# Kernel tuning notes

Measured on AMD Instinct MI355X. Metric: run time of the kernel, lower is better.

## Reference

```python
import jax, jax.numpy as jnp
import numpy as np

# --- constants mirroring init_kwargs ---
DIM = 1024
N_HEADS = 16
N_KV_HEADS = 4
HEAD_DIM = DIM // N_HEADS          # 64
REP = N_HEADS // N_KV_HEADS        # 4
ROPE_THETA = 10000.0
WINDOW = 512
N_GLOBAL = 64
EPS = 1e-6


def setup_inputs() -> dict:
    key = jax.random.key(0)
    ks = jax.random.split(key, 7)
    B, L = 2, 2048
    x = jax.random.normal(ks[0], (B, L, DIM), dtype=jnp.float32)
    s = 0.02
    wq = jax.random.normal(ks[1], (DIM, N_HEADS * HEAD_DIM), dtype=jnp.float32) * s
    wk = jax.random.normal(ks[2], (DIM, N_KV_HEADS * HEAD_DIM), dtype=jnp.float32) * s
    wv = jax.random.normal(ks[3], (DIM, N_KV_HEADS * HEAD_DIM), dtype=jnp.float32) * s
    wo = jax.random.normal(ks[4], (N_HEADS * HEAD_DIM, DIM), dtype=jnp.float32) * s
    gq = jnp.ones((HEAD_DIM,), dtype=jnp.float32) + 0.01 * jax.random.normal(ks[5], (HEAD_DIM,), dtype=jnp.float32)
    gk = jnp.ones((HEAD_DIM,), dtype=jnp.float32) + 0.01 * jax.random.normal(ks[6], (HEAD_DIM,), dtype=jnp.float32)
    return {"x": x, "wq": wq, "wk": wk, "wv": wv, "wo": wo, "gq": gq, "gk": gk}


def _rmsnorm(t, g):
    # QKNorm: RMS norm over head_dim with learnable per-dim scale
    return t * jax.lax.rsqrt(jnp.mean(t * t, axis=-1, keepdims=True) + EPS) * g


def _rope(t, cos, sin):
    # t: [B,H,L,hd]; complex RoPE over consecutive pairs (2i, 2i+1)
    t1 = t[..., 0::2]
    t2 = t[..., 1::2]
    o1 = t1 * cos - t2 * sin
    o2 = t1 * sin + t2 * cos
    return jnp.stack([o1, o2], axis=-1).reshape(t.shape)


def reference(x, wq, wk, wv, wo, gq, gk):
    B, L, D = x.shape
    q = (x @ wq).reshape(B, L, N_HEADS, HEAD_DIM)
    k = (x @ wk).reshape(B, L, N_KV_HEADS, HEAD_DIM)
    v = (x @ wv).reshape(B, L, N_KV_HEADS, HEAD_DIM)
    q = _rmsnorm(q, gq)
    k = _rmsnorm(k, gk)
    q = q.transpose(0, 2, 1, 3)  # [B,H,L,hd]
    k = k.transpose(0, 2, 1, 3)
    v = v.transpose(0, 2, 1, 3)

    # RoPE frequencies (start_pos = 0)
    inv_freq = 1.0 / (ROPE_THETA ** (jnp.arange(0, HEAD_DIM, 2, dtype=jnp.float32) / HEAD_DIM))
    ang = jnp.arange(L, dtype=jnp.float32)[:, None] * inv_freq[None, :]  # [L, hd/2]
    cos, sin = jnp.cos(ang), jnp.sin(ang)
    q = _rope(q, cos, sin)
    k = _rope(k, cos, sin)

    # GQA: repeat kv heads (repeat_interleave on head dim)
    k = jnp.repeat(k, REP, axis=1)
    v = jnp.repeat(v, REP, axis=1)

    scores = jnp.einsum("bhqd,bhkd->bhqk", q, k) / np.sqrt(HEAD_DIM).astype(np.float32)

    # sliding-window + global-token causal mask
    half = WINDOW // 2
    i = jnp.arange(L)[:, None]
    j = jnp.arange(L)[None, :]
    m = (j <= i) & ((j >= i - half) | (j < N_GLOBAL))  # [L,L] bool
    scores = jnp.where(m[None, None], scores, -jnp.inf)

    attn = jax.nn.softmax(scores.astype(jnp.float32), axis=-1).astype(scores.dtype)
    out = jnp.einsum("bhqk,bhkd->bhqd", attn, v)
    out = out.transpose(0, 2, 1, 3).reshape(B, L, N_HEADS * HEAD_DIM)
    return out @ wo
```

## Files before the change

kernel.cpp:

```cpp
#include <hip/hip_runtime.h>
#include <hip/hip_bf16.h>

typedef __bf16 bf16x8 __attribute__((ext_vector_type(8)));
typedef __bf16 bf16x4 __attribute__((ext_vector_type(4)));
typedef float  f32x4  __attribute__((ext_vector_type(4)));
typedef short  s16x4  __attribute__((ext_vector_type(4)));

__device__ __forceinline__ __bf16 to_bf16(float f) {
    __hip_bfloat16 h = __float2bfloat16(f);
    return *reinterpret_cast<__bf16*>(&h);
}

__device__ __forceinline__ f32x4 mfma32(bf16x8 a, bf16x8 b, f32x4 c) {
    return __builtin_amdgcn_mfma_f32_16x16x32_bf16(a, b, c, 0, 0, 0);
}
__device__ __forceinline__ f32x4 mfma16(bf16x4 a, bf16x4 b, f32x4 c) {
#if __has_builtin(__builtin_amdgcn_mfma_f32_16x16x16_bf16)
    return __builtin_amdgcn_mfma_f32_16x16x16_bf16(a, b, c, 0, 0, 0);
#else
    return __builtin_amdgcn_mfma_f32_16x16x16bf16_1k(
        __builtin_bit_cast(s16x4, a), __builtin_bit_cast(s16x4, b), c, 0, 0, 0);
#endif
}

__device__ __forceinline__ void gload_lds16(const __bf16* g, __bf16* l) {
    __builtin_amdgcn_global_load_lds(
        (const __attribute__((address_space(1))) void*)g,
        (__attribute__((address_space(3))) void*)l, 16, 0, 0);
}


__global__ __launch_bounds__(256) void prep_k(const float* __restrict__ wq,
                                              const float* __restrict__ wk,
                                              const float* __restrict__ wv,
                                              const float* __restrict__ wo,
                                              const float* __restrict__ x,
                                              __bf16* __restrict__ WqkvT,
                                              __bf16* __restrict__ WoT,
                                              __bf16* __restrict__ xb) {
    int b = blockIdx.x, tid = threadIdx.x;
    if (b >= 2560) {
        int i = ((b - 2560) * 256 + tid) * 8;
        f32x4 a = *(const f32x4*)(x + i);
        f32x4 c = *(const f32x4*)(x + i + 4);
        bf16x8 h;
        h[0] = to_bf16(a.x); h[1] = to_bf16(a.y); h[2] = to_bf16(a.z); h[3] = to_bf16(a.w);
        h[4] = to_bf16(c.x); h[5] = to_bf16(c.y); h[6] = to_bf16(c.z); h[7] = to_bf16(c.w);
        *(bf16x8*)(xb + i) = h;
        return;
    }
    __shared__ float tile[32][33];
    const float* src; __bf16* dst; int N, idx;
    if (b < 1024)      { src = wq; dst = WqkvT;                        N = 1024; idx = b; }
    else if (b < 1280) { src = wk; dst = WqkvT + (size_t)1024 * 1024;  N = 256;  idx = b - 1024; }
    else if (b < 1536) { src = wv; dst = WqkvT + (size_t)1280 * 1024;  N = 256;  idx = b - 1280; }
    else               { src = wo; dst = WoT;                          N = 1024; idx = b - 1536; }
    int k0 = (idx & 31) * 32, n0 = (idx >> 5) * 32;
    int tx = tid & 31, ty = tid >> 5;
#pragma unroll
    for (int r = 0; r < 4; ++r) {
        int kk = ty + r * 8;
        tile[kk][tx] = src[(size_t)(k0 + kk) * N + n0 + tx];
    }
    __syncthreads();
#pragma unroll
    for (int r = 0; r < 4; ++r) {
        int nn = ty + r * 8;
        dst[(size_t)(n0 + nn) * 1024 + k0 + tx] = to_bf16(tile[tx][nn]);
    }
}

#define GEMM_CORE(A, BT, K)                                                     \
    __shared__ __bf16 lA[8192];                                                 \
    __shared__ __bf16 lB[4096];                                                 \
    int tid = threadIdx.x;                                                      \
    int m0 = blockIdx.x * 128, n0 = blockIdx.y * 64;                            \
    int wid = tid >> 6, lane = tid & 63;                                        \
    int wm = (wid & 1) * 64, wn = (wid >> 1) * 32;                              \
    int lm = lane & 15, qd = lane >> 4;                                         \
    f32x4 acc[4][2] = {};                                                       \
    for (int k0 = 0; k0 < (K); k0 += 64) {                                      \
        _Pragma("unroll")                                                       \
        for (int it = 0; it < 4; ++it) {                                        \
            int kh = it >> 1, half = it & 1;                                    \
            int c = half * 256 + tid;                                           \
            int row = c >> 2, c4 = c & 3;                                       \
            __bf16* la = lA + kh * 4096 + half * 2048 + wid * 512;              \
            gload_lds16((A) + (size_t)(m0 + row) * (K) + k0 + kh * 32 + c4 * 8, la); \
        }                                                                       \
        _Pragma("unroll")                                                       \
        for (int kh = 0; kh < 2; ++kh) {                                        \
            int row = tid >> 2, c4 = tid & 3;                                   \
            __bf16* lb = lB + kh * 2048 + wid * 512;                            \
            gload_lds16((BT) + (size_t)(n0 + row) * (K) + k0 + kh * 32 + c4 * 8, lb); \
        }                                                                       \
        __syncthreads();                                                        \
        _Pragma("unroll")                                                       \
        for (int kh = 0; kh < 2; ++kh) {                                        \
            bf16x8 af[4], bfr[2];                                               \
            _Pragma("unroll")                                                   \
            for (int t = 0; t < 4; ++t) {                                       \
                int row = wm + t * 16 + lm;                                     \
                af[t] = *(const bf16x8*)&lA[kh * 4096 + (row >> 6) * 2048       \
                                            + (row & 63) * 32 + qd * 8];        \
            }                                                                   \
            _Pragma("unroll")                                                   \
            for (int j = 0; j < 2; ++j)                                         \
                bfr[j] = *(const bf16x8*)&lB[kh * 2048 + (wn + j * 16 + lm) * 32 \
                                             + qd * 8];                         \
            _Pragma("unroll")                                                   \
            for (int ti = 0; ti < 4; ++ti)                                      \
                _Pragma("unroll")                                               \
                for (int tj = 0; tj < 2; ++tj)                                  \
                    acc[ti][tj] = mfma32(af[ti], bfr[tj], acc[ti][tj]);         \
        }                                                                       \
        __syncthreads();                                                        \
    }

__global__ __launch_bounds__(256) void gemmqkv_k(const __bf16* __restrict__ A,
                                                 const __bf16* __restrict__ BT,
                                                 const float* __restrict__ gq,
                                                 const float* __restrict__ gk,
                                                 __bf16* __restrict__ Qb,
                                                 __bf16* __restrict__ Kbl,
                                                 __bf16* __restrict__ Vt) {
    __shared__ float ssp[2][128];
    __shared__ __bf16 tv[64 * 136];
    GEMM_CORE(A, BT, 1024)
    int head = n0 >> 6;

    if (head < 20) {
#pragma unroll
        for (int ti = 0; ti < 4; ++ti)
#pragma unroll
            for (int r = 0; r < 4; ++r) {
                float sq = acc[ti][0][r] * acc[ti][0][r] + acc[ti][1][r] * acc[ti][1][r];
                sq += __shfl_xor(sq, 1);
                sq += __shfl_xor(sq, 2);
                sq += __shfl_xor(sq, 4);
                sq += __shfl_xor(sq, 8);
                if (lm == 0) ssp[wid >> 1][wm + ti * 16 + qd * 4 + r] = sq;
            }
        __syncthreads();

        bool isq = head < 16;
#pragma unroll
        for (int ti = 0; ti < 4; ++ti)
#pragma unroll
            for (int r = 0; r < 4; ++r) {
                int row = wm + ti * 16 + qd * 4 + r;
                int t = m0 + row;
                int pos = t & 2047, bb = t >> 11;
                float ss = ssp[0][row] + ssp[1][row];
                float scale = rsqrtf(ss * (1.0f / 64.0f) + 1e-6f);
#pragma unroll
                for (int tj = 0; tj < 2; ++tj) {
                    int col = wn + tj * 16 + lm;
                    float g = isq ? gq[col] : gk[col];
                    float v = acc[ti][tj][r] * scale * g;
                    float ex = (float)(2 * (col >> 1)) * (1.0f / 64.0f);
                    float invf = expf(-ex * 9.210340371976184f);
                    float ang = (float)pos * invf;
                    float c = cosf(ang), s = sinf(ang);
                    float pv = __shfl_xor(v, 1);
                    float outv = (col & 1) ? (pv * s + v * c) : (v * c - pv * s);
                    if (isq) {
                        int kvh = head >> 2, h4 = head & 3;
                        size_t off = (((((size_t)bb * 4 + kvh) * 128 + (pos >> 4)) * 4 + h4) * 16
                                      + (pos & 15)) * 64 + col;
                        Qb[off] = to_bf16(outv * 0.125f);
                    } else {
                        int kvg = head - 16;
                        Kbl[(((size_t)bb * 4 + kvg) * 2048 + pos) * 64 + col] = to_bf16(outv);
                    }
                }
            }
    } else {
#pragma unroll
        for (int ti = 0; ti < 4; ++ti)
#pragma unroll
            for (int tj = 0; tj < 2; ++tj)
#pragma unroll
                for (int r = 0; r < 4; ++r) {
                    int row = wm + ti * 16 + qd * 4 + r;
                    int col = wn + tj * 16 + lm;
                    tv[col * 136 + row] = to_bf16(acc[ti][tj][r]);
                }
        __syncthreads();
        int bb = m0 >> 11, kvg = head - 20;
        size_t gg = (size_t)bb * 4 + kvg;
        int pos0 = m0 & 2047;
#pragma unroll
        for (int p = 0; p < 4; ++p) {
            int d = p * 16 + (tid >> 4);
            int tok = (tid & 15) * 8;
            bf16x8 vvv = *(const bf16x8*)&tv[d * 136 + tok];
            *(bf16x8*)(Vt + (gg * 64 + d) * 2048 + pos0 + tok) = vvv;
        }
    }
}

__global__ __launch_bounds__(256) void gemm_bf16_k(const __bf16* __restrict__ A,
                                                   const __bf16* __restrict__ BT,
                                                   float* __restrict__ C,
                                                   int K, int N) {
    GEMM_CORE(A, BT, K)
#pragma unroll
    for (int ti = 0; ti < 4; ++ti)
#pragma unroll
        for (int tj = 0; tj < 2; ++tj)
#pragma unroll
            for (int r = 0; r < 4; ++r) {
                int row = m0 + wm + ti * 16 + qd * 4 + r;
                int col = n0 + wn + tj * 16 + lm;
                C[(size_t)row * N + col] = acc[ti][tj][r];
            }
}

__global__ __launch_bounds__(512) void attn_k(const __bf16* __restrict__ Qb,
                                              const __bf16* __restrict__ Kbl,
                                              const __bf16* __restrict__ Vt,
                                              __bf16* __restrict__ aout) {
    __shared__ __bf16 Kt[2][64 * 64];
    __shared__ __bf16 Vl[2][64 * 64];
    int tid = threadIdx.x, wid = tid >> 6, lane = tid & 63;
    int l15 = lane & 15, quad = lane >> 4;
    int qb = blockIdx.x, kvh = blockIdx.y, b = blockIdx.z;
    int qg = wid >> 2;
    int h4 = wid & 3;
    int iw0 = qb * 32;
    int iw = iw0 + qg * 16;
    int g = b * 4 + kvh;
    int h = kvh * 4 + h4;
    int e7 = l15 & 7;

    int qbi = qb * 2 + qg;
    const __bf16* qp = Qb + ((((size_t)g * 128 + qbi) * 4 + h4) * 16 + l15) * 64 + quad * 8;
    bf16x8 qf0 = *(const bf16x8*)qp;
    bf16x8 qf1 = *(const bf16x8*)(qp + 32);

    int ts = (iw0 - 256) >> 6; if (ts < 1) ts = 1;
    int tmaxb = (iw0 + 31) >> 6;
    int n_all = (tmaxb >= ts) ? (tmaxb - ts + 2) : 1;
    int tmaxw = (iw + 15) >> 6;

    const __bf16* Kg = Kbl + (size_t)g * 2048 * 64;
    const __bf16* Vg = Vt + (size_t)g * 64 * 2048;

    int r0 = tid >> 3, c0 = tid & 7;
    int kl = r0 * 64 + ((c0 ^ (r0 & 7)) * 8);

    bf16x8 kr, vr;
    auto stage_load = [&](int tt) {
        kr = *(const bf16x8*)(Kg + (size_t)tt * 64 * 64 + r0 * 64 + c0 * 8);
        vr = *(const bf16x8*)(Vg + (size_t)r0 * 2048 + tt * 64 + c0 * 8);
    };
    auto stage_write = [&](int buf) {
        *(bf16x8*)&Kt[buf][kl] = kr;
        *(bf16x8*)&Vl[buf][kl] = vr;
    };

    stage_load(0);
    stage_write(0);

    f32x4 o[4] = {};
    float mr = -1e30f, lrp = 0.f;
    int iq = iw + l15;

    for (int idx = 0; idx < n_all; ++idx) {
        int tt = (idx == 0) ? 0 : ts + idx - 1;
        if (idx + 1 < n_all) stage_load(ts + idx);
        __syncthreads();
        int buf = idx & 1;

        f32x4 s[4] = {};
#pragma unroll
        for (int nt = 0; nt < 4; ++nt) {
            const __bf16* kp = &Kt[buf][(nt * 16 + l15) * 64];
            bf16x8 k0 = *(const bf16x8*)(kp + ((quad ^ e7) * 8));
            bf16x8 k1 = *(const bf16x8*)(kp + (((quad + 4) ^ e7) * 8));
            s[nt] = mfma32(k0, qf0, s[nt]);
            s[nt] = mfma32(k1, qf1, s[nt]);
        }

        bool need_mask = (tt >= tmaxw) || (tt >= 1 && tt * 64 < iw + 15 - 256);
        if (need_mask) {
#pragma unroll
            for (int nt = 0; nt < 4; ++nt)
#pragma unroll
                for (int r = 0; r < 4; ++r) {
                    int j = tt * 64 + nt * 16 + quad * 4 + r;
                    bool valid = (j <= iq) && ((j >= iq - 256) || (j < 64));
                    s[nt][r] = valid ? s[nt][r] : -1e30f;
                }
        }

        float mx = -1e30f;
#pragma unroll
        for (int nt = 0; nt < 4; ++nt)
#pragma unroll
            for (int r = 0; r < 4; ++r) mx = fmaxf(mx, s[nt][r]);
        mx = fmaxf(mx, __shfl_xor(mx, 16));
        mx = fmaxf(mx, __shfl_xor(mx, 32));
        float mn = fmaxf(mr, mx);
        float alpha = __expf(mr - mn);
        mr = mn;

        float ps = 0.f;
        bf16x4 pb[4];
#pragma unroll
        for (int nt = 0; nt < 4; ++nt)
#pragma unroll
            for (int r = 0; r < 4; ++r) {
                float pv = __expf(s[nt][r] - mn);
                ps += pv;
                pb[nt][r] = to_bf16(pv);
            }
        lrp = lrp * alpha + ps;

#pragma unroll
        for (int dt = 0; dt < 4; ++dt) {
            o[dt] *= alpha;
            const __bf16* vp = &Vl[buf][(dt * 16 + l15) * 64];
#pragma unroll
            for (int nt = 0; nt < 4; ++nt) {
                int c8 = 2 * nt + (quad >> 1);
                bf16x4 va = *(const bf16x4*)(vp + ((c8 ^ e7) * 8) + (quad & 1) * 4);
                o[dt] = mfma16(va, pb[nt], o[dt]);
            }
        }

        if (idx + 1 < n_all) stage_write((idx + 1) & 1);
    }

    lrp += __shfl_xor(lrp, 16);
    lrp += __shfl_xor(lrp, 32);
    float inv = 1.f / lrp;
    __syncthreads();
    __bf16* pr = (__bf16*)Kt + wid * 16 * 64;
#pragma unroll
    for (int dt = 0; dt < 4; ++dt)
#pragma unroll
        for (int r = 0; r < 4; ++r) {
            int e = dt * 16 + quad * 4 + r;
            int c8 = e >> 3;
            pr[l15 * 64 + ((c8 ^ e7) * 8) + (e & 7)] = to_bf16(o[dt][r] * inv);
        }
    bf16x8 o0 = *(const bf16x8*)(pr + l15 * 64 + (((2 * quad) ^ e7) * 8));
    bf16x8 o1 = *(const bf16x8*)(pr + l15 * 64 + (((2 * quad + 1) ^ e7) * 8));
    __bf16* op = aout + ((size_t)b * 2048 + iw + l15) * 1024 + h * 64 + quad * 16;
    *(bf16x8*)op = o0;
    *(bf16x8*)(op + 8) = o1;
}

extern "C" void kernel_launch(void* const* d_in, const int* in_sizes, int n_in,
                              void* d_out, int out_size, void* d_ws, size_t ws_size,
                              hipStream_t stream) {
    const float* x  = (const float*)d_in[0];
    const float* wq = (const float*)d_in[1];
    const float* wk = (const float*)d_in[2];
    const float* wv = (const float*)d_in[3];
    const float* wo = (const float*)d_in[4];
    const float* gq = (const float*)d_in[5];
    const float* gk = (const float*)d_in[6];
    float* out = (float*)d_out;

    char* ws = (char*)d_ws;
    __bf16* WqkvT = (__bf16*)ws;
    __bf16* WoT   = (__bf16*)(ws + 3145728);
    __bf16* xb_ao = (__bf16*)(ws + 5242880);
    __bf16* Kbl   = (__bf16*)(ws + 13631488);
    __bf16* Vt    = (__bf16*)(ws + 15728640);
    __bf16* Qb    = (__bf16*)(ws + 17825792);

    dim3 tb(256);
    prep_k<<<4608, tb, 0, stream>>>(wq, wk, wv, wo, x, WqkvT, WoT, xb_ao);
    gemmqkv_k<<<dim3(32, 24), tb, 0, stream>>>(xb_ao, WqkvT, gq, gk, Qb, Kbl, Vt);
    attn_k<<<dim3(64, 4, 2), dim3(512), 0, stream>>>(Qb, Kbl, Vt, xb_ao);
    gemm_bf16_k<<<dim3(32, 16), tb, 0, stream>>>(xb_ao, WoT, out, 1024, 1024);
}
```

Baseline: 151.0 us.

## Widen GEMM tiles to 128x128 and precompute RoPE cos/sin table

The shared GEMM core now computes 128x128 output tiles instead of 128x64, so each warp covers a full 64-wide head. That halves the grid for both the QKV and output projections and raises MFMA work per LDS load. With a full head per warp, the QK-norm reduction happens in registers via shuffles, with no shared-memory partial sums or barrier. RoPE cos/sin values are precomputed into a table inside the prep kernel instead of calling expf/cosf/sinf per element in the epilogue. The cost is fewer blocks (384 and 256), which may underfill the GPU's CUs, plus more accumulator registers per thread.

```diff
diff --git a/kernel.cpp b/kernel.cpp
--- a/kernel.cpp
+++ b/kernel.cpp
@@ -37,8 +37,18 @@
                                               const float* __restrict__ x,
                                               __bf16* __restrict__ WqkvT,
                                               __bf16* __restrict__ WoT,
-                                              __bf16* __restrict__ xb) {
+                                              __bf16* __restrict__ xb,
+                                              float2* __restrict__ rope_tab) {
     int b = blockIdx.x, tid = threadIdx.x;
+    if (b >= 4608) {
+        int idx = (b - 4608) * 256 + tid;
+        int pos = idx >> 5, f = idx & 31;
+        float ex = (float)(2 * f) * (1.0f / 64.0f);
+        float invf = expf(-ex * 9.210340371976184f);
+        float ang = (float)pos * invf;
+        rope_tab[idx] = make_float2(cosf(ang), sinf(ang));
+        return;
+    }
     if (b >= 2560) {
         int i = ((b - 2560) * 256 + tid) * 8;
         f32x4 a = *(const f32x4*)(x + i);
@@ -70,48 +80,44 @@
     }
 }
 
-#define GEMM_CORE(A, BT, K)                                                     \
-    __shared__ __bf16 lA[8192];                                                 \
-    __shared__ __bf16 lB[4096];                                                 \
+#define GEMM_CORE128(A, BT, K)                                                  \
+    __shared__ __bf16 smem[16384];                                              \
+    __bf16* lA = smem;                                                          \
+    __bf16* lB = smem + 8192;                                                   \
     int tid = threadIdx.x;                                                      \
-    int m0 = blockIdx.x * 128, n0 = blockIdx.y * 64;                            \
+    int m0 = blockIdx.x * 128, n0 = blockIdx.y * 128;                           \
     int wid = tid >> 6, lane = tid & 63;                                        \
-    int wm = (wid & 1) * 64, wn = (wid >> 1) * 32;                              \
+    int wm = (wid & 1) * 64, wn = (wid >> 1) * 64;                              \
     int lm = lane & 15, qd = lane >> 4;                                         \
-    f32x4 acc[4][2] = {};                                                       \
+    f32x4 acc[4][4] = {};                                                       \
     for (int k0 = 0; k0 < (K); k0 += 64) {                                      \
         _Pragma("unroll")                                                       \
         for (int it = 0; it < 4; ++it) {                                        \
             int kh = it >> 1, half = it & 1;                                    \
             int c = half * 256 + tid;                                           \
             int row = c >> 2, c4 = c & 3;                                       \
-            __bf16* la = lA + kh * 4096 + half * 2048 + wid * 512;              \
-            gload_lds16((A) + (size_t)(m0 + row) * (K) + k0 + kh * 32 + c4 * 8, la); \
-        }                                                                       \
-        _Pragma("unroll")                                                       \
-        for (int kh = 0; kh < 2; ++kh) {                                        \
-            int row = tid >> 2, c4 = tid & 3;                                   \
-            __bf16* lb = lB + kh * 2048 + wid * 512;                            \
-            gload_lds16((BT) + (size_t)(n0 + row) * (K) + k0 + kh * 32 + c4 * 8, lb); \
+            __bf16* ldst = lA + kh * 4096 + half * 2048 + wid * 512;            \
+            gload_lds16((A) + (size_t)(m0 + row) * (K) + k0 + kh * 32 + c4 * 8, ldst); \
+            __bf16* ldstb = lB + kh * 4096 + half * 2048 + wid * 512;           \
+            gload_lds16((BT) + (size_t)(n0 + row) * (K) + k0 + kh * 32 + c4 * 8, ldstb); \
         }                                                                       \
         __syncthreads();                                                        \
         _Pragma("unroll")                                                       \
         for (int kh = 0; kh < 2; ++kh) {                                        \
-            bf16x8 af[4], bfr[2];                                               \
+            bf16x8 af[4], bfr[4];                                               \
             _Pragma("unroll")                                                   \
             for (int t = 0; t < 4; ++t) {                                       \
                 int row = wm + t * 16 + lm;                                     \
                 af[t] = *(const bf16x8*)&lA[kh * 4096 + (row >> 6) * 2048       \
                                             + (row & 63) * 32 + qd * 8];        \
+                int col = wn + t * 16 + lm;                                     \
+                bfr[t] = *(const bf16x8*)&lB[kh * 4096 + (col >> 6) * 2048      \
+                                             + (col & 63) * 32 + qd * 8];       \
             }                                                                   \
-            _Pragma("unroll")                                                   \
-            for (int j = 0; j < 2; ++j)                                         \
-                bfr[j] = *(const bf16x8*)&lB[kh * 2048 + (wn + j * 16 + lm) * 32 \
-                                             + qd * 8];                         \
             _Pragma("unroll")                                                   \
             for (int ti = 0; ti < 4; ++ti)                                      \
                 _Pragma("unroll")                                               \
-                for (int tj = 0; tj < 2; ++tj)                                  \
+                for (int tj = 0; tj < 4; ++tj)                                  \
                     acc[ti][tj] = mfma32(af[ti], bfr[tj], acc[ti][tj]);         \
         }                                                                       \
         __syncthreads();                                                        \
@@ -119,31 +125,22 @@
 
 __global__ __launch_bounds__(256) void gemmqkv_k(const __bf16* __restrict__ A,
                                                  const __bf16* __restrict__ BT,
+                                                 const float2* __restrict__ rope_tab,
                                                  const float* __restrict__ gq,
                                                  const float* __restrict__ gk,
                                                  __bf16* __restrict__ Qb,
                                                  __bf16* __restrict__ Kbl,
                                                  __bf16* __restrict__ Vt) {
-    __shared__ float ssp[2][128];
-    __shared__ __bf16 tv[64 * 136];
-    GEMM_CORE(A, BT, 1024)
-    int head = n0 >> 6;
-
-    if (head < 20) {
-#pragma unroll
-        for (int ti = 0; ti < 4; ++ti)
-#pragma unroll
-            for (int r = 0; r < 4; ++r) {
-                float sq = acc[ti][0][r] * acc[ti][0][r] + acc[ti][1][r] * acc[ti][1][r];
-                sq += __shfl_xor(sq, 1);
-                sq += __shfl_xor(sq, 2);
-                sq += __shfl_xor(sq, 4);
-                sq += __shfl_xor(sq, 8);
-                if (lm == 0) ssp[wid >> 1][wm + ti * 16 + qd * 4 + r] = sq;
-            }
-        __syncthreads();
-
+    GEMM_CORE128(A, BT, 1024)
+    int head0 = n0 >> 6;
+
+    if (head0 < 20) {
+        int head = head0 + (wn >> 6);
         bool isq = head < 16;
+        const float* gvec = isq ? gq : gk;
+        float gam[4];
+#pragma unroll
+        for (int tj = 0; tj < 4; ++tj) gam[tj] = gvec[tj * 16 + lm];
 #pragma unroll
         for (int ti = 0; ti < 4; ++ti)
 #pragma unroll
@@ -151,51 +148,59 @@
                 int row = wm + ti * 16 + qd * 4 + r;
                 int t = m0 + row;
                 int pos = t & 2047, bb = t >> 11;
-                float ss = ssp[0][row] + ssp[1][row];
+                float ss = acc[ti][0][r] * acc[ti][0][r] + acc[ti][1][r] * acc[ti][1][r]
+                         + acc[ti][2][r] * acc[ti][2][r] + acc[ti][3][r] * acc[ti][3][r];
+                ss += __shfl_xor(ss, 1);
+                ss += __shfl_xor(ss, 2);
+                ss += __shfl_xor(ss, 4);
+                ss += __shfl_xor(ss, 8);
                 float scale = rsqrtf(ss * (1.0f / 64.0f) + 1e-6f);
 #pragma unroll
-                for (int tj = 0; tj < 2; ++tj) {
-                    int col = wn + tj * 16 + lm;
-                    float g = isq ? gq[col] : gk[col];
-                    float v = acc[ti][tj][r] * scale * g;
-                    float ex = (float)(2 * (col >> 1)) * (1.0f / 64.0f);
-                    float invf = expf(-ex * 9.210340371976184f);
-                    float ang = (float)pos * invf;
-                    float c = cosf(ang), s = sinf(ang);
+                for (int tj = 0; tj < 4; ++tj) {
+                    int cw = tj * 16 + lm;
+                    float v = acc[ti][tj][r] * scale * gam[tj];
+                    float2 cs = rope_tab[pos * 32 + (cw >> 1)];
                     float pv = __shfl_xor(v, 1);
-                    float outv = (col & 1) ? (pv * s + v * c) : (v * c - pv * s);
+                    float outv = (cw & 1) ? (pv * cs.y + v * cs.x) : (v * cs.x - pv * cs.y);
                     if (isq) {
                         int kvh = head >> 2, h4 = head & 3;
                         size_t off = (((((size_t)bb * 4 + kvh) * 128 + (pos >> 4)) * 4 + h4) * 16
-                                      + (pos & 15)) * 64 + col;
+                                      + (pos & 15)) * 64 + cw;
                         Qb[off] = to_bf16(outv * 0.125f);
                     } else {
                         int kvg = head - 16;
-                        Kbl[(((size_t)bb * 4 + kvg) * 2048 + pos) * 64 + col] = to_bf16(outv);
+                        Kbl[(((size_t)bb * 4 + kvg) * 2048 + pos) * 64 + cw] = to_bf16(outv);
                     }
                 }
             }
     } else {
-#pragma unroll
-        for (int ti = 0; ti < 4; ++ti)
-#pragma unroll
-            for (int tj = 0; tj < 2; ++tj)
-#pragma unroll
-                for (int r = 0; r < 4; ++r) {
-                    int row = wm + ti * 16 + qd * 4 + r;
-                    int col = wn + tj * 16 + lm;
-                    tv[col * 136 + row] = to_bf16(acc[ti][tj][r]);
-                }
-        __syncthreads();
-        int bb = m0 >> 11, kvg = head - 20;
-        size_t gg = (size_t)bb * 4 + kvg;
-        int pos0 = m0 & 2047;
-#pragma unroll
-        for (int p = 0; p < 4; ++p) {
-            int d = p * 16 + (tid >> 4);
-            int tok = (tid & 15) * 8;
-            bf16x8 vvv = *(const bf16x8*)&tv[d * 136 + tok];
-            *(bf16x8*)(Vt + (gg * 64 + d) * 2048 + pos0 + tok) = vvv;
+        __bf16* tv = smem;
+        int bb = m0 >> 11, pos0 = m0 & 2047;
+#pragma unroll
+        for (int hh = 0; hh < 2; ++hh) {
+            if ((wn >> 6) == hh) {
+#pragma unroll
+                for (int ti = 0; ti < 4; ++ti)
+#pragma unroll
+                    for (int tj = 0; tj < 4; ++tj)
+#pragma unroll
+                        for (int r = 0; r < 4; ++r) {
+                            int row = wm + ti * 16 + qd * 4 + r;
+                            int cw = tj * 16 + lm;
+                            tv[cw * 136 + row] = to_bf16(acc[ti][tj][r]);
+                        }
+            }
+            __syncthreads();
+            int kvg = head0 + hh - 20;
+            size_t gg = (size_t)bb * 4 + kvg;
+#pragma unroll
+            for (int p = 0; p < 4; ++p) {
+                int d = p * 16 + (tid >> 4);
+                int tok = (tid & 15) * 8;
+                bf16x8 vvv = *(const bf16x8*)&tv[d * 136 + tok];
+                *(bf16x8*)(Vt + (gg * 64 + d) * 2048 + pos0 + tok) = vvv;
+            }
+            __syncthreads();
         }
     }
 }
@@ -204,11 +209,11 @@
                                                    const __bf16* __restrict__ BT,
                                                    float* __restrict__ C,
                                                    int K, int N) {
-    GEMM_CORE(A, BT, K)
+    GEMM_CORE128(A, BT, K)
 #pragma unroll
     for (int ti = 0; ti < 4; ++ti)
 #pragma unroll
-        for (int tj = 0; tj < 2; ++tj)
+        for (int tj = 0; tj < 4; ++tj)
 #pragma unroll
             for (int r = 0; r < 4; ++r) {
                 int row = m0 + wm + ti * 16 + qd * 4 + r;
@@ -366,16 +371,17 @@
     float* out = (float*)d_out;
 
     char* ws = (char*)d_ws;
-    __bf16* WqkvT = (__bf16*)ws;
-    __bf16* WoT   = (__bf16*)(ws + 3145728);
-    __bf16* xb_ao = (__bf16*)(ws + 5242880);
-    __bf16* Kbl   = (__bf16*)(ws + 13631488);
-    __bf16* Vt    = (__bf16*)(ws + 15728640);
-    __bf16* Qb    = (__bf16*)(ws + 17825792);
+    __bf16*  WqkvT = (__bf16*)ws;
+    __bf16*  WoT   = (__bf16*)(ws + 3145728);
+    __bf16*  xb_ao = (__bf16*)(ws + 5242880);
+    __bf16*  Kbl   = (__bf16*)(ws + 13631488);
+    __bf16*  Vt    = (__bf16*)(ws + 15728640);
+    __bf16*  Qb    = (__bf16*)(ws + 17825792);
+    float2*  rtab  = (float2*)(ws + 26214400);
 
     dim3 tb(256);
-    prep_k<<<4608, tb, 0, stream>>>(wq, wk, wv, wo, x, WqkvT, WoT, xb_ao);
-    gemmqkv_k<<<dim3(32, 24), tb, 0, stream>>>(xb_ao, WqkvT, gq, gk, Qb, Kbl, Vt);
+    prep_k<<<4864, tb, 0, stream>>>(wq, wk, wv, wo, x, WqkvT, WoT, xb_ao, rtab);
+    gemmqkv_k<<<dim3(32, 12), tb, 0, stream>>>(xb_ao, WqkvT, rtab, gq, gk, Qb, Kbl, Vt);
     attn_k<<<dim3(64, 4, 2), dim3(512), 0, stream>>>(Qb, Kbl, Vt, xb_ao);
-    gemm_bf16_k<<<dim3(32, 16), tb, 0, stream>>>(xb_ao, WoT, out, 1024, 1024);
-}
+    gemm_bf16_k<<<dim3(32, 8), tb, 0, stream>>>(xb_ao, WoT, out, 1024, 1024);
+}
```

After: 148.4 us. No clear change (-1.7%).
